# Kernel optimization log

Hardware: AMD Instinct MI355X
Metric: run time of the kernel (lower is better)

Reference implementation:

```python
import jax, jax.numpy as jnp
import numpy as np

B, N, L, D = 256, 128, 2048, 64
ATOM_V, AMINO_V = 2000, 10000
LAYER_GNN, LAYER_CNN, LAYER_OUT = 3, 3, 2
SIDE = 5
WINDOW = 2 * SIDE + 1   # 11 -> conv kernel 23x23, padding 11
N_OUT = 2
EPS = 1e-6


def setup_inputs() -> dict:
    ks = jax.random.split(jax.random.key(0), 16)
    s = 0.05
    return {
        "atoms": jax.random.randint(ks[0], (B, N), 0, ATOM_V),
        "atoms_mask": jnp.ones((B, N), jnp.float32),
        "adjacency": jax.random.uniform(ks[1], (B, N, N), jnp.float32),
        "amino": jax.random.randint(ks[2], (B, L), 0, AMINO_V),
        "amino_mask": jnp.ones((B, L), jnp.float32),
        "emb_fp": jax.random.normal(ks[3], (ATOM_V, D), jnp.float32) * s,
        "emb_word": jax.random.normal(ks[4], (AMINO_V, D), jnp.float32) * s,
        "W_gnn": jax.random.normal(ks[5], (LAYER_GNN, D, D), jnp.float32) * s,
        "b_gnn": jax.random.normal(ks[6], (LAYER_GNN, D), jnp.float32) * s,
        "conv_k": jax.random.normal(ks[7], (LAYER_CNN, 2 * WINDOW + 1, 2 * WINDOW + 1), jnp.float32) * s,
        "conv_b": jax.random.normal(ks[8], (LAYER_CNN,), jnp.float32) * s,
        "W_att": jax.random.normal(ks[9], (D, D), jnp.float32) * s,
        "b_att": jax.random.normal(ks[10], (D,), jnp.float32) * s,
        "W_out": jax.random.normal(ks[11], (LAYER_OUT, 2 * D, 2 * D), jnp.float32) * s,
        "b_out": jax.random.normal(ks[12], (LAYER_OUT, 2 * D), jnp.float32) * s,
        "W_int": jax.random.normal(ks[13], (N_OUT, 2 * D), jnp.float32) * s,
        "b_int": jax.random.normal(ks[14], (N_OUT,), jnp.float32) * s,
    }


def reference(atoms, atoms_mask, adjacency, amino, amino_mask,
              emb_fp, emb_word, W_gnn, b_gnn, conv_k, conv_b,
              W_att, b_att, W_out, b_out, W_int, b_int):
    # ---- compound vector via GNN over dense adjacency ----
    xs = emb_fp[atoms]                                   # [B,N,D]
    for i in range(LAYER_GNN):
        hs = jax.nn.relu(jnp.einsum('bnd,ed->bne', xs, W_gnn[i]) + b_gnn[i])
        xs = xs + jnp.einsum('bnm,bmd->bnd', adjacency, hs)
    am = atoms_mask[..., None]                           # [B,N,1]
    compound = (jnp.sum(xs * am, axis=1) / (jnp.sum(am, axis=1) + EPS))[:, None, :]  # [B,1,D]

    # ---- protein vector via attention-CNN ----
    ps = emb_word[amino][:, None]                        # [B,1,L,D] (NCHW)
    for i in range(LAYER_CNN):
        y = jax.lax.conv_general_dilated(
            ps, conv_k[i][None, None], (1, 1),
            [(WINDOW, WINDOW), (WINDOW, WINDOW)],
            dimension_numbers=('NCHW', 'OIHW', 'NCHW'))
        ps = jax.nn.relu(y + conv_b[i])
    ps = ps[:, 0]                                        # [B,L,D]
    h = jax.nn.relu(jnp.einsum('bqd,ed->bqe', compound, W_att) + b_att)  # [B,1,D]
    hs = jax.nn.relu(jnp.einsum('bld,ed->ble', ps, W_att) + b_att)       # [B,L,D]
    pm = amino_mask[..., None]                           # [B,L,1]
    hs = hs * pm
    weights = jnp.tanh(jnp.einsum('bqd,bld->bql', h, hs))  # [B,1,L]
    ys = jnp.transpose(weights, (0, 2, 1)) * hs             # [B,L,D]
    protein = (jnp.sum(ys, axis=1) / (jnp.sum(pm, axis=1) + EPS))[:, None, :]  # [B,1,D]

    # ---- fuse and predict ----
    cat = jnp.concatenate([compound, protein], axis=2)[:, 0]  # [B,2D]
    for j in range(LAYER_OUT):
        cat = jax.nn.relu(cat @ W_out[j].T + b_out[j])  # dropout is identity in eval
    return cat @ W_int.T + b_int                          # [B,N_OUT]
```

## Files before the change

### kernel.cpp

```cpp
#include <hip/hip_runtime.h>
#include <hip/hip_bf16.h>
#include <cstdint>
#include <cstddef>

#define BB 256
#define NN 128
#define LL 2048
#define DD 64
#define KS 23
#define CPAD 12
#define EPSF 1e-6f
#define ACH 8

typedef __bf16 v8bf __attribute__((ext_vector_type(8)));
typedef float v4f __attribute__((ext_vector_type(4)));

__device__ __forceinline__ float bf2f(uint32_t u) {
  union { uint32_t i; float f; } c; c.i = u << 16; return c.f;
}
__device__ __forceinline__ uint16_t f2bf(float f) {
  union { float f; uint32_t i; } c; c.f = f;
  uint32_t i = c.i;
  return (uint16_t)((i + 0x7fffu + ((i >> 16) & 1u)) >> 16);
}
__device__ __forceinline__ v8bf cvt8(float4 f0, float4 f1) {
  v8bf r;
  r[0] = (__bf16)f0.x; r[1] = (__bf16)f0.y; r[2] = (__bf16)f0.z; r[3] = (__bf16)f0.w;
  r[4] = (__bf16)f1.x; r[5] = (__bf16)f1.y; r[6] = (__bf16)f1.z; r[7] = (__bf16)f1.w;
  return r;
}

#define XSS 68
#define HTS3 136

__global__ __launch_bounds__(512) void gnn_kernel(
    const int* __restrict__ atoms, const float* __restrict__ atoms_mask,
    const float* __restrict__ adj, const float* __restrict__ emb_fp,
    const float* __restrict__ W_gnn, const float* __restrict__ b_gnn,
    const float* __restrict__ W_att, const float* __restrict__ b_att,
    const float* __restrict__ conv_k, uint16_t* __restrict__ btab,
    float* __restrict__ compound, float* __restrict__ hvec_g)
{
  __shared__ float xs[NN * XSS];
  __shared__ uint16_t hsT[DD * HTS3];
  __shared__ float mask_s[NN];
  __shared__ float psum[8][64];
  __shared__ float cvec[64];

  const int b = blockIdx.x;
  const int tid = threadIdx.x;
  const int lane = tid & 63;
  const int w = tid >> 6;
  const int m16 = lane & 15;
  const int s = lane >> 4;

  for (int idx = tid; idx < NN * 16; idx += 512) {
    int n = idx >> 4, c4 = idx & 15;
    int a = atoms[b * NN + n];
    float4 v = ((const float4*)(emb_fp + (size_t)a * DD))[c4];
    *(float4*)(xs + n * XSS + c4 * 4) = v;
  }
  if (tid < NN) mask_s[tid] = atoms_mask[b * NN + tid];
  __syncthreads();

  const int row0 = 16 * w;
  for (int layer = 0; layer < 3; ++layer) {
    v8bf Wf[2][4];
    float bias[4];
    const float* Wl = W_gnn + (size_t)layer * DD * DD;
    #pragma unroll
    for (int nt = 0; nt < 4; ++nt) {
      bias[nt] = b_gnn[layer * DD + nt * 16 + m16];
      #pragma unroll
      for (int kc = 0; kc < 2; ++kc) {
        const float* p = Wl + (size_t)(nt * 16 + m16) * DD + kc * 32 + s * 8;
        Wf[kc][nt] = cvt8(((const float4*)p)[0], ((const float4*)p)[1]);
      }
    }
    float4 araw[4][2];
    const float* adjw = adj + ((size_t)b * NN + row0 + m16) * NN;
    #pragma unroll
    for (int kc = 0; kc < 4; ++kc) {
      const float* p = adjw + kc * 32 + s * 8;
      araw[kc][0] = ((const float4*)p)[0];
      araw[kc][1] = ((const float4*)p)[1];
    }

    v4f acc[4];
    #pragma unroll
    for (int nt = 0; nt < 4; ++nt)
      acc[nt] = (v4f){bias[nt], bias[nt], bias[nt], bias[nt]};
    #pragma unroll
    for (int kc = 0; kc < 2; ++kc) {
      const float* p = xs + (size_t)(row0 + m16) * XSS + kc * 32 + s * 8;
      v8bf Axs = cvt8(((const float4*)p)[0], ((const float4*)p)[1]);
      #pragma unroll
      for (int nt = 0; nt < 4; ++nt)
        acc[nt] = __builtin_amdgcn_mfma_f32_16x16x32_bf16(
            Axs, Wf[kc][nt], acc[nt], 0, 0, 0);
    }
    __syncthreads();
    #pragma unroll
    for (int nt = 0; nt < 4; ++nt) {
      int e = nt * 16 + m16;
      int m = row0 + s * 4;
      union { uint64_t u; __bf16 h[4]; } pk;
      #pragma unroll
      for (int r = 0; r < 4; ++r)
        pk.h[r] = (__bf16)fmaxf(acc[nt][r], 0.f);
      *(uint64_t*)(hsT + (size_t)e * HTS3 + m) = pk.u;
    }
    __syncthreads();

    v4f acc2[4];
    #pragma unroll
    for (int nt = 0; nt < 4; ++nt)
      #pragma unroll
      for (int r = 0; r < 4; ++r)
        acc2[nt][r] = xs[(size_t)(row0 + s * 4 + r) * XSS + nt * 16 + m16];
    #pragma unroll
    for (int kc = 0; kc < 4; ++kc) {
      v8bf Aa = cvt8(araw[kc][0], araw[kc][1]);
      v8bf Bh[4];
      #pragma unroll
      for (int nt = 0; nt < 4; ++nt)
        Bh[nt] = *(const v8bf*)(hsT + (size_t)(nt * 16 + m16) * HTS3 + kc * 32 + s * 8);
      #pragma unroll
      for (int nt = 0; nt < 4; ++nt)
        acc2[nt] = __builtin_amdgcn_mfma_f32_16x16x32_bf16(
            Aa, Bh[nt], acc2[nt], 0, 0, 0);
    }
    #pragma unroll
    for (int nt = 0; nt < 4; ++nt)
      #pragma unroll
      for (int r = 0; r < 4; ++r)
        xs[(size_t)(row0 + s * 4 + r) * XSS + nt * 16 + m16] = acc2[nt][r];
  }

  float pr = 0.f;
  for (int i = 0; i < 16; ++i) {
    int n = row0 + i;
    pr = fmaf(mask_s[n], xs[(size_t)n * XSS + lane], pr);
  }
  psum[w][lane] = pr;
  __syncthreads();
  if (tid < 64) {
    float ssum = 0.f;
    #pragma unroll
    for (int k = 0; k < 8; ++k) ssum += psum[k][tid];
    float den = 0.f;
    #pragma unroll 8
    for (int i = 0; i < NN; ++i) den += mask_s[i];
    float c = ssum / (den + EPSF);
    compound[b * DD + tid] = c;
    cvec[tid] = c;
  }
  __syncthreads();
  if (tid < 64) {
    float a = b_att[tid];
    const float* wr = W_att + (size_t)tid * DD;
    #pragma unroll
    for (int d4 = 0; d4 < 16; ++d4) {
      float4 w4 = ((const float4*)wr)[d4];
      float4 c4 = ((const float4*)cvec)[d4];
      a = fmaf(w4.x, c4.x, a); a = fmaf(w4.y, c4.y, a);
      a = fmaf(w4.z, c4.z, a); a = fmaf(w4.w, c4.w, a);
    }
    hvec_g[b * DD + tid] = fmaxf(a, 0.f);
  }

  if (b < 3) {
    for (int kk = w; kk < 30; kk += 8) {
      int k8 = kk * 4 + s;
      int i = k8 / 5;
      int c8k = k8 - i * 5;
      #pragma unroll
      for (int j = 0; j < 8; ++j) {
        int c = c8k * 8 + j;
        int jj = c - m16 - 1;
        float v = (i < KS && jj >= 0 && jj < KS)
                      ? conv_k[b * KS * KS + i * KS + jj] : 0.f;
        btab[(((size_t)b * 30 + kk) * 64 + lane) * 8 + j] = f2bf(v);
      }
    }
  }
}

#define TW 88
#define TROWS 86

__global__ __launch_bounds__(256, 2) void conv_kernel(
    const uint16_t* __restrict__ in, uint16_t* __restrict__ out,
    const uint16_t* __restrict__ btab, const float* __restrict__ conv_b,
    const int* __restrict__ amino, const float* __restrict__ emb_word,
    int layer, int gmode)
{
  __shared__ uint16_t tile[TROWS * TW];
  const int tid = threadIdx.x;
  const int l0 = blockIdx.x * 64;
  const int b  = blockIdx.y;
  const int lane = tid & 63;
  const int g = tid >> 6;

  v8bf bfr[29];
  const uint16_t* bt = btab + (size_t)layer * 30 * 512 + lane * 8;
  #pragma unroll
  for (int kk = 0; kk < 29; ++kk)
    bfr[kk] = *(const v8bf*)(bt + kk * 512);

  for (int i = tid; i < TROWS * 6; i += 256) {
    int r = i / 6, h = i - r * 6;
    int off = (h < 3) ? h * 4 : 76 + (h - 3) * 4;
    *(uint2*)(tile + r * TW + off) = make_uint2(0u, 0u);
  }
  const uint16_t* inb = in + (size_t)b * LL * DD;
  for (int idx = tid; idx < TROWS * 8; idx += 256) {
    int t = idx >> 3, c8 = idx & 7;
    int gl = l0 - 11 + t;
    uint16_t* dst = tile + t * TW + CPAD + c8 * 8;
    if (gl >= 0 && gl < LL) {
      if (gmode) {
        int a = amino[b * LL + gl];
        const float* src = emb_word + (size_t)a * DD + c8 * 8;
        float4 f0 = ((const float4*)src)[0];
        float4 f1 = ((const float4*)src)[1];
        union { uint2 u2[2]; uint16_t h[8]; } pk;
        pk.h[0] = f2bf(f0.x); pk.h[1] = f2bf(f0.y);
        pk.h[2] = f2bf(f0.z); pk.h[3] = f2bf(f0.w);
        pk.h[4] = f2bf(f1.x); pk.h[5] = f2bf(f1.y);
        pk.h[6] = f2bf(f1.z); pk.h[7] = f2bf(f1.w);
        *(uint2*)(dst)     = pk.u2[0];
        *(uint2*)(dst + 4) = pk.u2[1];
      } else {
        uint4 v = *(const uint4*)(inb + (size_t)gl * DD + c8 * 8);
        *(uint2*)(dst)     = make_uint2(v.x, v.y);
        *(uint2*)(dst + 4) = make_uint2(v.z, v.w);
      }
    } else {
      *(uint2*)(dst)     = make_uint2(0u, 0u);
      *(uint2*)(dst + 4) = make_uint2(0u, 0u);
    }
  }
  __syncthreads();

  const int s = lane >> 4;
  const int m16 = lane & 15;
  v4f acc[4];
  #pragma unroll
  for (int m = 0; m < 4; ++m) acc[m] = (v4f){0.f, 0.f, 0.f, 0.f};

  #pragma unroll
  for (int kk = 0; kk < 29; ++kk) {
    int k8 = kk * 4 + s;
    int i = k8 / 5;
    int c8 = k8 - i * 5;
    const uint16_t* ap = tile + (m16 + i) * TW + 16 * g + c8 * 8;
    v8bf a0 = *(const v8bf*)(ap);
    v8bf a1 = *(const v8bf*)(ap + 16 * TW);
    v8bf a2 = *(const v8bf*)(ap + 32 * TW);
    v8bf a3 = *(const v8bf*)(ap + 48 * TW);
    acc[0] = __builtin_amdgcn_mfma_f32_16x16x32_bf16(a0, bfr[kk], acc[0], 0, 0, 0);
    acc[1] = __builtin_amdgcn_mfma_f32_16x16x32_bf16(a1, bfr[kk], acc[1], 0, 0, 0);
    acc[2] = __builtin_amdgcn_mfma_f32_16x16x32_bf16(a2, bfr[kk], acc[2], 0, 0, 0);
    acc[3] = __builtin_amdgcn_mfma_f32_16x16x32_bf16(a3, bfr[kk], acc[3], 0, 0, 0);
  }

  const float bias = conv_b[layer];
  uint16_t* outb = out + ((size_t)b * LL + l0) * DD + 16 * g + m16;
  #pragma unroll
  for (int m = 0; m < 4; ++m) {
    #pragma unroll
    for (int r = 0; r < 4; ++r) {
      int row = m * 16 + s * 4 + r;
      outb[(size_t)row * DD] = f2bf(fmaxf(acc[m][r] + bias, 0.f));
    }
  }
}

#define HTS2 66

__global__ __launch_bounds__(256) void attn_part_kernel(
    const uint16_t* __restrict__ ps, const float* __restrict__ amino_mask,
    const float* __restrict__ hvec_g, const float* __restrict__ W_att,
    const float* __restrict__ b_att, float* __restrict__ pacc_part,
    float* __restrict__ msum_part)
{
  __shared__ float ht[4][32 * HTS2];
  __shared__ float pm_s[4][64];
  __shared__ float wv_s[4][32];
  __shared__ float hv_s[64];

  const int chunk = blockIdx.x;
  const int b = blockIdx.y;
  const int tid = threadIdx.x;
  const int lane = tid & 63;
  const int w = tid >> 6;
  const int m16 = lane & 15;
  const int s = lane >> 4;

  v8bf bfrB[2][4];
  float bias[4];
  #pragma unroll
  for (int nt = 0; nt < 4; ++nt) {
    bias[nt] = b_att[nt * 16 + m16];
    const float* wr = W_att + (size_t)(nt * 16 + m16) * DD + s * 8;
    #pragma unroll
    for (int kc = 0; kc < 2; ++kc) {
      float4 f0 = ((const float4*)(wr + kc * 32))[0];
      float4 f1 = ((const float4*)(wr + kc * 32))[1];
      bfrB[kc][nt] = cvt8(f0, f1);
    }
  }
  if (tid < 64) hv_s[tid] = hvec_g[b * DD + tid];

  const int rowbase = chunk * 256 + w * 64;
  const float* pmb = amino_mask + (size_t)b * LL;
  pm_s[w][lane] = pmb[rowbase + lane];
  const float macc = pm_s[w][lane];
  __syncthreads();

  float pacc[4] = {0.f, 0.f, 0.f, 0.f};
  const uint16_t* psb = ps + ((size_t)b * LL + rowbase) * DD;

  #pragma unroll
  for (int step = 0; step < 2; ++step) {
    const uint16_t* pr = psb + (size_t)step * 32 * DD;
    v8bf A[2][2];
    #pragma unroll
    for (int mt = 0; mt < 2; ++mt)
      #pragma unroll
      for (int kc = 0; kc < 2; ++kc)
        A[mt][kc] = *(const v8bf*)(pr + (mt * 16 + m16) * DD + kc * 32 + s * 8);

    v4f acc[2][4];
    #pragma unroll
    for (int mt = 0; mt < 2; ++mt)
      #pragma unroll
      for (int nt = 0; nt < 4; ++nt)
        acc[mt][nt] = (v4f){0.f, 0.f, 0.f, 0.f};
    #pragma unroll
    for (int kc = 0; kc < 2; ++kc)
      #pragma unroll
      for (int mt = 0; mt < 2; ++mt)
        #pragma unroll
        for (int nt = 0; nt < 4; ++nt)
          acc[mt][nt] = __builtin_amdgcn_mfma_f32_16x16x32_bf16(
              A[mt][kc], bfrB[kc][nt], acc[mt][nt], 0, 0, 0);

    float vals[2][4][4];
    float* htw = ht[w];
    #pragma unroll
    for (int mt = 0; mt < 2; ++mt)
      #pragma unroll
      for (int r = 0; r < 4; ++r) {
        int row = mt * 16 + s * 4 + r;
        float pm = pm_s[w][step * 32 + row];
        #pragma unroll
        for (int nt = 0; nt < 4; ++nt) {
          float v = fmaxf(acc[mt][nt][r] + bias[nt], 0.f) * pm;
          vals[mt][nt][r] = v;
          htw[row * HTS2 + nt * 16 + m16] = v;
        }
      }
    __syncthreads();

    {
      int row = lane & 31, eh = lane >> 5;
      const float* hr = ht[w] + row * HTS2 + eh * 32;
      const float* hv = hv_s + eh * 32;
      float d = 0.f;
      #pragma unroll
      for (int t = 0; t < 8; ++t) {
        float4 hh = *(const float4*)(hr + 4 * t);
        float4 vv = *(const float4*)(hv + 4 * t);
        d = fmaf(hh.x, vv.x, d); d = fmaf(hh.y, vv.y, d);
        d = fmaf(hh.z, vv.z, d); d = fmaf(hh.w, vv.w, d);
      }
      d += __shfl_xor(d, 32);
      float wt = tanhf(d);
      if (lane < 32) wv_s[w][row] = wt;
    }
    __syncthreads();

    #pragma unroll
    for (int mt = 0; mt < 2; ++mt)
      #pragma unroll
      for (int r = 0; r < 4; ++r) {
        float wt = wv_s[w][mt * 16 + s * 4 + r];
        #pragma unroll
        for (int nt = 0; nt < 4; ++nt)
          pacc[nt] = fmaf(wt, vals[mt][nt][r], pacc[nt]);
      }
    __syncthreads();
  }

  const size_t idx = ((size_t)b * ACH + chunk) * 4 + w;
  #pragma unroll
  for (int nt = 0; nt < 4; ++nt) {
    float p = pacc[nt];
    p += __shfl_xor(p, 16);
    p += __shfl_xor(p, 32);
    if (m16 == lane)
      pacc_part[idx * 64 + nt * 16 + lane] = p;
  }
  float m = macc;
  #pragma unroll
  for (int off = 1; off < 64; off <<= 1) m += __shfl_xor(m, off);
  if (lane == 0) msum_part[idx] = m;
}

__global__ __launch_bounds__(128) void attn_final_kernel(
    const float* __restrict__ compound, const float* __restrict__ pacc_part,
    const float* __restrict__ msum_part, const float* __restrict__ W_out,
    const float* __restrict__ b_out, const float* __restrict__ W_int,
    const float* __restrict__ b_int, float* __restrict__ outp)
{
  __shared__ float cat[128];
  __shared__ float cat2[128];
  const int b = blockIdx.x;
  const int tid = threadIdx.x;

  if (tid < 64) {
    float p = 0.f, den = 0.f;
    #pragma unroll 4
    for (int c = 0; c < ACH * 4; ++c) {
      p += pacc_part[((size_t)b * ACH * 4 + c) * 64 + tid];
      den += msum_part[b * ACH * 4 + c];
    }
    cat[tid] = compound[b * DD + tid];
    cat[64 + tid] = p / (den + EPSF);
  }
  __syncthreads();
  {
    float a = b_out[tid];
    const float* wr = W_out + (size_t)tid * 128;
    #pragma unroll 8
    for (int dd = 0; dd < 128; ++dd) a = fmaf(wr[dd], cat[dd], a);
    cat2[tid] = fmaxf(a, 0.f);
  }
  __syncthreads();
  {
    float a = b_out[128 + tid];
    const float* wr = W_out + 128 * 128 + (size_t)tid * 128;
    #pragma unroll 8
    for (int dd = 0; dd < 128; ++dd) a = fmaf(wr[dd], cat2[dd], a);
    __syncthreads();
    cat[tid] = fmaxf(a, 0.f);
  }
  __syncthreads();
  if (tid < 2) {
    float a = b_int[tid];
    const float* wr = W_int + (size_t)tid * 128;
    #pragma unroll 8
    for (int dd = 0; dd < 128; ++dd) a = fmaf(wr[dd], cat[dd], a);
    outp[b * 2 + tid] = a;
  }
}

extern "C" void kernel_launch(void* const* d_in, const int* in_sizes, int n_in,
                              void* d_out, int out_size, void* d_ws, size_t ws_size,
                              hipStream_t stream) {
  const int*   atoms      = (const int*)d_in[0];
  const float* atoms_mask = (const float*)d_in[1];
  const float* adjacency  = (const float*)d_in[2];
  const int*   amino      = (const int*)d_in[3];
  const float* amino_mask = (const float*)d_in[4];
  const float* emb_fp     = (const float*)d_in[5];
  const float* emb_word   = (const float*)d_in[6];
  const float* W_gnn      = (const float*)d_in[7];
  const float* b_gnn      = (const float*)d_in[8];
  const float* conv_k     = (const float*)d_in[9];
  const float* conv_b     = (const float*)d_in[10];
  const float* W_att      = (const float*)d_in[11];
  const float* b_att      = (const float*)d_in[12];
  const float* W_out      = (const float*)d_in[13];
  const float* b_out      = (const float*)d_in[14];
  const float* W_int      = (const float*)d_in[15];
  const float* b_int      = (const float*)d_in[16];
  float* out = (float*)d_out;

  char* ws = (char*)d_ws;
  const size_t ps_bytes = (size_t)BB * LL * DD * 2;
  float*    compound  = (float*)ws;
  uint16_t* ps_a      = (uint16_t*)(ws + 65536);
  uint16_t* ps_b      = (uint16_t*)(ws + 65536 + ps_bytes);
  uint16_t* btab      = (uint16_t*)(ws + 65536 + 2 * ps_bytes);
  float*    hvec_g    = (float*)(ws + 65536 + 2 * ps_bytes + 131072);
  float*    pacc_part = (float*)ps_a;
  float*    msum_part = (float*)((char*)ps_a + (size_t)BB * ACH * 4 * 64 * 4);

  gnn_kernel<<<BB, 512, 0, stream>>>(atoms, atoms_mask, adjacency, emb_fp,
                                     W_gnn, b_gnn, W_att, b_att,
                                     conv_k, btab, compound, hvec_g);
  conv_kernel<<<dim3(32, BB), 256, 0, stream>>>(ps_a, ps_b, btab, conv_b,
                                                amino, emb_word, 0, 1);
  conv_kernel<<<dim3(32, BB), 256, 0, stream>>>(ps_b, ps_a, btab, conv_b,
                                                amino, emb_word, 1, 0);
  conv_kernel<<<dim3(32, BB), 256, 0, stream>>>(ps_a, ps_b, btab, conv_b,
                                                amino, emb_word, 2, 0);
  attn_part_kernel<<<dim3(ACH, BB), 256, 0, stream>>>(ps_b, amino_mask, hvec_g,
                                                      W_att, b_att,
                                                      pacc_part, msum_part);
  attn_final_kernel<<<BB, 128, 0, stream>>>(compound, pacc_part, msum_part,
                                            W_out, b_out, W_int, b_int, out);
}
```

Measured before the change: 374.9 us.

## Switch conv to 32x32x16 MFMA with 128-row tiles and streamed Toeplitz B

The conv kernel now uses 32x32x16 bf16 MFMA instead of 16x16x32, with a rebuilt banded B table of 81 chunks. Each block covers 128 sequence rows instead of 64, and the B fragments are loaded in three passes of 27 rather than all held in registers. Larger tiles cut the halo overhead per output row, and the bigger MFMA shape needs fewer LDS reads per FLOP. The change adds register pressure and extra B-table traffic, and the Toeplitz padding grows from 29 to 81 k-chunks. Separately, the GNN kernel converts the adjacency rows to bf16 once and keeps them across layers instead of reloading them each layer.

```diff
diff --git a/kernel.cpp b/kernel.cpp
--- a/kernel.cpp
+++ b/kernel.cpp
@@ -11,9 +11,11 @@
 #define CPAD 12
 #define EPSF 1e-6f
 #define ACH 8
+#define NCH 81
 
 typedef __bf16 v8bf __attribute__((ext_vector_type(8)));
 typedef float v4f __attribute__((ext_vector_type(4)));
+typedef float v16f __attribute__((ext_vector_type(16)));
 
 __device__ __forceinline__ float bf2f(uint32_t u) {
   union { uint32_t i; float f; } c; c.i = u << 16; return c.f;
@@ -38,7 +40,7 @@
     const float* __restrict__ adj, const float* __restrict__ emb_fp,
     const float* __restrict__ W_gnn, const float* __restrict__ b_gnn,
     const float* __restrict__ W_att, const float* __restrict__ b_att,
-    const float* __restrict__ conv_k, uint16_t* __restrict__ btab,
+    const float* __restrict__ conv_k, uint16_t* __restrict__ btab2,
     float* __restrict__ compound, float* __restrict__ hvec_g)
 {
   __shared__ float xs[NN * XSS];
@@ -54,6 +56,17 @@
   const int m16 = lane & 15;
   const int s = lane >> 4;
 
+  const int row0 = 16 * w;
+  v8bf adjf[4];
+  {
+    const float* adjw = adj + ((size_t)b * NN + row0 + m16) * NN;
+    #pragma unroll
+    for (int kc = 0; kc < 4; ++kc) {
+      const float* p = adjw + kc * 32 + s * 8;
+      adjf[kc] = cvt8(((const float4*)p)[0], ((const float4*)p)[1]);
+    }
+  }
+
   for (int idx = tid; idx < NN * 16; idx += 512) {
     int n = idx >> 4, c4 = idx & 15;
     int a = atoms[b * NN + n];
@@ -63,7 +76,6 @@
   if (tid < NN) mask_s[tid] = atoms_mask[b * NN + tid];
   __syncthreads();
 
-  const int row0 = 16 * w;
   for (int layer = 0; layer < 3; ++layer) {
     v8bf Wf[2][4];
     float bias[4];
@@ -77,14 +89,6 @@
         Wf[kc][nt] = cvt8(((const float4*)p)[0], ((const float4*)p)[1]);
       }
     }
-    float4 araw[4][2];
-    const float* adjw = adj + ((size_t)b * NN + row0 + m16) * NN;
-    #pragma unroll
-    for (int kc = 0; kc < 4; ++kc) {
-      const float* p = adjw + kc * 32 + s * 8;
-      araw[kc][0] = ((const float4*)p)[0];
-      araw[kc][1] = ((const float4*)p)[1];
-    }
 
     v4f acc[4];
     #pragma unroll
@@ -120,7 +124,6 @@
         acc2[nt][r] = xs[(size_t)(row0 + s * 4 + r) * XSS + nt * 16 + m16];
     #pragma unroll
     for (int kc = 0; kc < 4; ++kc) {
-      v8bf Aa = cvt8(araw[kc][0], araw[kc][1]);
       v8bf Bh[4];
       #pragma unroll
       for (int nt = 0; nt < 4; ++nt)
@@ -128,7 +131,7 @@
       #pragma unroll
       for (int nt = 0; nt < 4; ++nt)
         acc2[nt] = __builtin_amdgcn_mfma_f32_16x16x32_bf16(
-            Aa, Bh[nt], acc2[nt], 0, 0, 0);
+            adjf[kc], Bh[nt], acc2[nt], 0, 0, 0);
     }
     #pragma unroll
     for (int nt = 0; nt < 4; ++nt)
@@ -170,51 +173,46 @@
   }
 
   if (b < 3) {
-    for (int kk = w; kk < 30; kk += 8) {
-      int k8 = kk * 4 + s;
-      int i = k8 / 5;
-      int c8k = k8 - i * 5;
+    const int n32 = lane & 31;
+    const int sh = lane >> 5;
+    for (int kk = w; kk < NCH; kk += 8) {
+      int k8 = 2 * kk + sh;
+      int i = k8 / 7;
+      int c8v = k8 - 7 * i;
       #pragma unroll
       for (int j = 0; j < 8; ++j) {
-        int c = c8k * 8 + j;
-        int jj = c - m16 - 1;
+        int jj = c8v * 8 + j - n32 - 1;
         float v = (i < KS && jj >= 0 && jj < KS)
                       ? conv_k[b * KS * KS + i * KS + jj] : 0.f;
-        btab[(((size_t)b * 30 + kk) * 64 + lane) * 8 + j] = f2bf(v);
+        btab2[(((size_t)b * NCH + kk) * 64 + lane) * 8 + j] = f2bf(v);
       }
     }
   }
 }
 
 #define TW 88
-#define TROWS 86
+#define TR2 150
 
 __global__ __launch_bounds__(256, 2) void conv_kernel(
     const uint16_t* __restrict__ in, uint16_t* __restrict__ out,
-    const uint16_t* __restrict__ btab, const float* __restrict__ conv_b,
+    const uint16_t* __restrict__ btab2, const float* __restrict__ conv_b,
     const int* __restrict__ amino, const float* __restrict__ emb_word,
     int layer, int gmode)
 {
-  __shared__ uint16_t tile[TROWS * TW];
+  __shared__ uint16_t tile[TR2 * TW];
   const int tid = threadIdx.x;
-  const int l0 = blockIdx.x * 64;
+  const int l0 = blockIdx.x * 128;
   const int b  = blockIdx.y;
   const int lane = tid & 63;
   const int g = tid >> 6;
 
-  v8bf bfr[29];
-  const uint16_t* bt = btab + (size_t)layer * 30 * 512 + lane * 8;
-  #pragma unroll
-  for (int kk = 0; kk < 29; ++kk)
-    bfr[kk] = *(const v8bf*)(bt + kk * 512);
-
-  for (int i = tid; i < TROWS * 6; i += 256) {
+  for (int i = tid; i < TR2 * 6; i += 256) {
     int r = i / 6, h = i - r * 6;
     int off = (h < 3) ? h * 4 : 76 + (h - 3) * 4;
     *(uint2*)(tile + r * TW + off) = make_uint2(0u, 0u);
   }
   const uint16_t* inb = in + (size_t)b * LL * DD;
-  for (int idx = tid; idx < TROWS * 8; idx += 256) {
+  for (int idx = tid; idx < TR2 * 8; idx += 256) {
     int t = idx >> 3, c8 = idx & 7;
     int gl = l0 - 11 + t;
     uint16_t* dst = tile + t * TW + CPAD + c8 * 8;
@@ -243,37 +241,44 @@
   }
   __syncthreads();
 
-  const int s = lane >> 4;
-  const int m16 = lane & 15;
-  v4f acc[4];
-  #pragma unroll
-  for (int m = 0; m < 4; ++m) acc[m] = (v4f){0.f, 0.f, 0.f, 0.f};
-
-  #pragma unroll
-  for (int kk = 0; kk < 29; ++kk) {
-    int k8 = kk * 4 + s;
-    int i = k8 / 5;
-    int c8 = k8 - i * 5;
-    const uint16_t* ap = tile + (m16 + i) * TW + 16 * g + c8 * 8;
-    v8bf a0 = *(const v8bf*)(ap);
-    v8bf a1 = *(const v8bf*)(ap + 16 * TW);
-    v8bf a2 = *(const v8bf*)(ap + 32 * TW);
-    v8bf a3 = *(const v8bf*)(ap + 48 * TW);
-    acc[0] = __builtin_amdgcn_mfma_f32_16x16x32_bf16(a0, bfr[kk], acc[0], 0, 0, 0);
-    acc[1] = __builtin_amdgcn_mfma_f32_16x16x32_bf16(a1, bfr[kk], acc[1], 0, 0, 0);
-    acc[2] = __builtin_amdgcn_mfma_f32_16x16x32_bf16(a2, bfr[kk], acc[2], 0, 0, 0);
-    acc[3] = __builtin_amdgcn_mfma_f32_16x16x32_bf16(a3, bfr[kk], acc[3], 0, 0, 0);
+  const int n32 = lane & 31;
+  const int sh = lane >> 5;
+  const int dg = g & 1;
+  const int mh = g >> 1;
+  const uint16_t* bt = btab2 + (size_t)layer * NCH * 512 + lane * 8;
+
+  v16f acc0, acc1;
+  #pragma unroll
+  for (int r = 0; r < 16; ++r) { acc0[r] = 0.f; acc1[r] = 0.f; }
+
+  #pragma unroll
+  for (int pass = 0; pass < 3; ++pass) {
+    v8bf Bf[27];
+    #pragma unroll
+    for (int t = 0; t < 27; ++t)
+      Bf[t] = *(const v8bf*)(bt + (size_t)(pass * 27 + t) * 512);
+    #pragma unroll
+    for (int t = 0; t < 27; ++t) {
+      int k8 = 2 * (pass * 27 + t) + sh;
+      int i = k8 / 7;
+      if (i > 22) i = 22;
+      int c8v = k8 - 7 * ((2 * (pass * 27 + t) + sh) / 7);
+      c8v = (2 * (pass * 27 + t) + sh) - 7 * ((2 * (pass * 27 + t) + sh) / 7);
+      const uint16_t* ap = tile + (size_t)(64 * mh + n32 + i) * TW + 32 * dg + c8v * 8;
+      v8bf a0 = *(const v8bf*)(ap);
+      v8bf a1 = *(const v8bf*)(ap + 32 * TW);
+      acc0 = __builtin_amdgcn_mfma_f32_32x32x16_bf16(a0, Bf[t], acc0, 0, 0, 0);
+      acc1 = __builtin_amdgcn_mfma_f32_32x32x16_bf16(a1, Bf[t], acc1, 0, 0, 0);
+    }
   }
 
   const float bias = conv_b[layer];
-  uint16_t* outb = out + ((size_t)b * LL + l0) * DD + 16 * g + m16;
-  #pragma unroll
-  for (int m = 0; m < 4; ++m) {
-    #pragma unroll
-    for (int r = 0; r < 4; ++r) {
-      int row = m * 16 + s * 4 + r;
-      outb[(size_t)row * DD] = f2bf(fmaxf(acc[m][r] + bias, 0.f));
-    }
+  uint16_t* outb = out + ((size_t)b * LL + l0 + 64 * mh) * DD + 32 * dg + n32;
+  #pragma unroll
+  for (int reg = 0; reg < 16; ++reg) {
+    int row = (reg & 3) + 8 * (reg >> 2) + 4 * sh;
+    outb[(size_t)row * DD]        = f2bf(fmaxf(acc0[reg] + bias, 0.f));
+    outb[(size_t)(32 + row) * DD] = f2bf(fmaxf(acc1[reg] + bias, 0.f));
   }
 }
 
@@ -484,19 +489,19 @@
   float*    compound  = (float*)ws;
   uint16_t* ps_a      = (uint16_t*)(ws + 65536);
   uint16_t* ps_b      = (uint16_t*)(ws + 65536 + ps_bytes);
-  uint16_t* btab      = (uint16_t*)(ws + 65536 + 2 * ps_bytes);
-  float*    hvec_g    = (float*)(ws + 65536 + 2 * ps_bytes + 131072);
+  uint16_t* btab2     = (uint16_t*)(ws + 65536 + 2 * ps_bytes);
+  float*    hvec_g    = (float*)(ws + 65536 + 2 * ps_bytes + 262144);
   float*    pacc_part = (float*)ps_a;
   float*    msum_part = (float*)((char*)ps_a + (size_t)BB * ACH * 4 * 64 * 4);
 
   gnn_kernel<<<BB, 512, 0, stream>>>(atoms, atoms_mask, adjacency, emb_fp,
                                      W_gnn, b_gnn, W_att, b_att,
-                                     conv_k, btab, compound, hvec_g);
-  conv_kernel<<<dim3(32, BB), 256, 0, stream>>>(ps_a, ps_b, btab, conv_b,
+                                     conv_k, btab2, compound, hvec_g);
+  conv_kernel<<<dim3(16, BB), 256, 0, stream>>>(ps_a, ps_b, btab2, conv_b,
                                                 amino, emb_word, 0, 1);
-  conv_kernel<<<dim3(32, BB), 256, 0, stream>>>(ps_b, ps_a, btab, conv_b,
+  conv_kernel<<<dim3(16, BB), 256, 0, stream>>>(ps_b, ps_a, btab2, conv_b,
                                                 amino, emb_word, 1, 0);
-  conv_kernel<<<dim3(32, BB), 256, 0, stream>>>(ps_a, ps_b, btab, conv_b,
+  conv_kernel<<<dim3(16, BB), 256, 0, stream>>>(ps_a, ps_b, btab2, conv_b,
                                                 amino, emb_word, 2, 0);
   attn_part_kernel<<<dim3(ACH, BB), 256, 0, stream>>>(ps_b, amino_mask, hvec_g,
                                                       W_att, b_att,
```

Result: slower. 414.8 us (+10.6%).
